# Performance work log

Hardware: AMD Instinct MI355X
Metric: run time of the kernel (lower is better)

Reference implementation:

```python
import jax, jax.numpy as jnp
import numpy as np

B, T, D, H = 8, 512, 1024, 16
DH = D // H  # per-head feature dim (64)


def setup_inputs() -> dict:
    key = jax.random.key(0)
    ks = jax.random.split(key, 10)
    s = 1.0 / np.sqrt(DH)
    inp = {
        "X_data": jax.random.normal(ks[0], (B, T, D), dtype=jnp.float32),
        "mask": jnp.ones((B, T), dtype=jnp.int32),
        # per-head Q/K/V projections (each SelfAttention has its own d_h x d_h weights)
        "Wq": jax.random.normal(ks[1], (H, DH, DH), dtype=jnp.float32) * s,
        "bq": jnp.zeros((H, DH), dtype=jnp.float32),
        "Wk": jax.random.normal(ks[2], (H, DH, DH), dtype=jnp.float32) * s,
        "bk": jnp.zeros((H, DH), dtype=jnp.float32),
        "Wv": jax.random.normal(ks[3], (H, DH, DH), dtype=jnp.float32) * s,
        "bv": jnp.zeros((H, DH), dtype=jnp.float32),
        # AttentionFusion: linear on concatenated head outputs -> len_feature_new
        "Wf": jax.random.normal(ks[4], (D, D), dtype=jnp.float32) * (1.0 / np.sqrt(D)),
        "bf": jnp.zeros((D,), dtype=jnp.float32),
    }
    return inp


def reference(X_data, mask, Wq, bq, Wk, bk, Wv, bv, Wf, bf):
    # Split features into heads: [B, T, H, DH] (equal partitions since D % H == 0)
    Xh = X_data.reshape(B, T, H, DH)
    # Batched per-head projections (replaces the Python loop over heads)
    Q = jnp.einsum("bthd,hde->bhte", Xh, Wq) + bq[None, :, None, :]
    K = jnp.einsum("bthd,hde->bhte", Xh, Wk) + bk[None, :, None, :]
    V = jnp.einsum("bthd,hde->bhte", Xh, Wv) + bv[None, :, None, :]
    scale = 1.0 / jnp.sqrt(jnp.asarray(DH, dtype=Q.dtype))
    scores = jnp.einsum("bhqe,bhke->bhqk", Q, K) * scale  # [B, H, T, T]
    scores = jnp.where(mask[:, None, None, :] > 0, scores, jnp.asarray(-1e9, scores.dtype))
    att = jax.nn.softmax(scores, axis=-1)
    out = jnp.einsum("bhqk,bhke->bhqe", att, V)  # [B, H, T, DH]
    # Concatenate heads (same order as the per-head loop) and fuse
    out = out.transpose(0, 2, 1, 3).reshape(B, T, D)
    fused = out @ Wf + bf  # AttentionFusion linear
    return fused
```

## Files before the change

### kernel.cpp

```cpp
#include <hip/hip_runtime.h>
#include <math.h>

#define B 8
#define T 512
#define D 1024
#define H 16
#define DH 64

typedef __bf16 bf16;
typedef __attribute__((ext_vector_type(8))) __bf16 bf16x8;
typedef __attribute__((ext_vector_type(4))) __bf16 bf16x4;
typedef __attribute__((ext_vector_type(4))) float f32x4;

__device__ __forceinline__ void gld16(const void* g, void* l) {
    __builtin_amdgcn_global_load_lds(
        (const __attribute__((address_space(1))) void*)g,
        (__attribute__((address_space(3))) void*)l, 16, 0, 0);
}


#define EXP2SCALE 1.44269504088896f

__global__ __launch_bounds__(256, 2) void qkv_attn(
    const float* __restrict__ X, const int* __restrict__ mask,
    const float* __restrict__ Wq, const float* __restrict__ Wk,
    const float* __restrict__ Wv,
    const float* __restrict__ bq, const float* __restrict__ bv,
    const float* __restrict__ Wf, bf16* __restrict__ WfT,
    bf16* __restrict__ Ob)
{
    __shared__ __align__(16) char smem[61952];

    if (blockIdx.x >= 512) {
        bf16* Ts = (bf16*)smem;
        const int ti = blockIdx.x - 512, tid = threadIdx.x;
        const int k0 = (ti >> 4) * 64, n0 = (ti & 15) * 64;
        for (int i = tid; i < 1024; i += 256) {
            const int k = i >> 4, nq = (i & 15) * 4;
            const float4 w = *(const float4*)(Wf + (size_t)(k0 + k) * D + n0 + nq);
            Ts[(nq + 0) * 72 + k] = (bf16)w.x; Ts[(nq + 1) * 72 + k] = (bf16)w.y;
            Ts[(nq + 2) * 72 + k] = (bf16)w.z; Ts[(nq + 3) * 72 + k] = (bf16)w.w;
        }
        __syncthreads();
        for (int i = tid; i < 512; i += 256) {
            const int n = i >> 3, kc = (i & 7) * 8;
            *(bf16x8*)(WfT + (size_t)(n0 + n) * D + k0 + kc) = *(const bf16x8*)&Ts[n * 72 + kc];
        }
        return;
    }

    bf16* Wvs  = (bf16*)(smem);
    bf16* Pl   = (bf16*)(smem + 43008);
    int*  msk  = (int*)(smem + 61440);
    bf16* Wqs  = (bf16*)(smem + 8192);
    bf16* WksT = (bf16*)(smem + 24576);
    bf16* Xq   = Pl;
    bf16* Stage = Pl;
    bf16* Ostage = Pl;

    const int bh = blockIdx.x & 127, q0 = (blockIdx.x >> 7) * 128;
    const int b = bh >> 4, h = bh & 15;
    const int tid = threadIdx.x, wave = tid >> 6, lane = tid & 63;
    const int quad = lane >> 4, l15 = lane & 15;

    const int pkrow = wave * 16 + (lane >> 2);
    const int pc0 = (lane & 3) * 2;

    float bqr[4], bvr[4];
#pragma unroll
    for (int nt = 0; nt < 4; ++nt) {
        bqr[nt] = bq[h * DH + nt * 16 + l15];
        bvr[nt] = bv[h * DH + nt * 16 + l15];
    }

    float4 px0, px1, px2, px3;
    {
        const float* src = X + (size_t)(b * T + pkrow) * D + h * DH + pc0 * 8;
        px0 = *(const float4*)src; px1 = *(const float4*)(src + 4);
        px2 = *(const float4*)(src + 8); px3 = *(const float4*)(src + 12);
    }
    int mreg = (tid < 64) ? mask[(size_t)b * T + tid] : 0;

    for (int i = tid; i < 1024; i += 256) {
        const int d = i >> 4, eq4 = (i & 15) * 4;
        const float4 wq4 = *(const float4*)(Wq + (size_t)h * 4096 + d * 64 + eq4);
        const float4 wk4 = *(const float4*)(Wk + (size_t)h * 4096 + d * 64 + eq4);
        const float4 wv4 = *(const float4*)(Wv + (size_t)h * 4096 + d * 64 + eq4);
#pragma unroll
        for (int j = 0; j < 4; ++j) {
            const int e = eq4 + j;
            const int idx = e * 64 + (((d >> 3) ^ (e & 7)) * 8) + (d & 7);
            Wqs[idx] = (bf16)((const float*)&wq4)[j];
            Wvs[idx] = (bf16)((const float*)&wv4)[j];
        }
        bf16x4 wkp;
        wkp[0] = (bf16)wk4.x; wkp[1] = (bf16)wk4.y;
        wkp[2] = (bf16)wk4.z; wkp[3] = (bf16)wk4.w;
        *(bf16x4*)&WksT[d * 64 + (((eq4 >> 3) ^ (d & 7)) * 8) + (eq4 & 7)] = wkp;
    }
    for (int i = tid; i < 1024; i += 256) {
        const int row = i >> 3, c = i & 7;
        const float* src = X + (size_t)(b * T + q0 + row) * D + h * DH + c * 8;
        const float4 x0 = *(const float4*)src;
        const float4 x1 = *(const float4*)(src + 4);
        bf16x8 t;
        t[0] = (bf16)x0.x; t[1] = (bf16)x0.y; t[2] = (bf16)x0.z; t[3] = (bf16)x0.w;
        t[4] = (bf16)x1.x; t[5] = (bf16)x1.y; t[6] = (bf16)x1.z; t[7] = (bf16)x1.w;
        *(bf16x8*)&Xq[row * 64 + ((c ^ (row & 7)) * 8)] = t;
    }
    __syncthreads();

    {
        f32x4 accQ[2][4] = {};
#pragma unroll
        for (int ks = 0; ks < 2; ++ks) {
            bf16x8 af[2], bfr[4];
#pragma unroll
            for (int mt = 0; mt < 2; ++mt) {
                const int row = wave * 32 + mt * 16 + l15;
                af[mt] = *(const bf16x8*)&Xq[row * 64 + (((ks * 4 + quad) ^ (l15 & 7)) * 8)];
            }
#pragma unroll
            for (int nt = 0; nt < 4; ++nt)
                bfr[nt] = *(const bf16x8*)&Wqs[(nt * 16 + l15) * 64 + (((ks * 4 + quad) ^ (l15 & 7)) * 8)];
#pragma unroll
            for (int mt = 0; mt < 2; ++mt)
#pragma unroll
                for (int nt = 0; nt < 4; ++nt)
                    accQ[mt][nt] = __builtin_amdgcn_mfma_f32_16x16x32_bf16(af[mt], bfr[nt], accQ[mt][nt], 0, 0, 0);
        }
        __syncthreads();
        const float qs = 0.125f * EXP2SCALE;
#pragma unroll
        for (int mt = 0; mt < 2; ++mt)
#pragma unroll
            for (int nt = 0; nt < 4; ++nt)
#pragma unroll
                for (int reg = 0; reg < 4; ++reg)
                    Stage[(wave * 32 + mt * 16 + quad * 4 + reg) * 72 + nt * 16 + l15] =
                        (bf16)((accQ[mt][nt][reg] + bqr[nt]) * qs);
        __builtin_amdgcn_wave_barrier();
    }
    bf16x8 qf[2][2];
#pragma unroll
    for (int mt = 0; mt < 2; ++mt)
#pragma unroll
        for (int ks = 0; ks < 2; ++ks)
            qf[mt][ks] = *(const bf16x8*)&Stage[(wave * 32 + mt * 16 + l15) * 72 + ks * 32 + quad * 8];

    bf16x8 qmf[2][2];
    {
        f32x4 accM[2][4] = {};
#pragma unroll
        for (int ks = 0; ks < 2; ++ks)
#pragma unroll
            for (int nt = 0; nt < 4; ++nt) {
                const bf16x8 wk8 = *(const bf16x8*)&WksT[(nt * 16 + l15) * 64 + (((ks * 4 + quad) ^ (l15 & 7)) * 8)];
#pragma unroll
                for (int mt = 0; mt < 2; ++mt)
                    accM[mt][nt] = __builtin_amdgcn_mfma_f32_16x16x32_bf16(wk8, qf[mt][ks], accM[mt][nt], 0, 0, 0);
            }
        __builtin_amdgcn_wave_barrier();
#pragma unroll
        for (int mt = 0; mt < 2; ++mt)
#pragma unroll
            for (int nt = 0; nt < 4; ++nt) {
                bf16x4 qp;
#pragma unroll
                for (int reg = 0; reg < 4; ++reg) qp[reg] = (bf16)accM[mt][nt][reg];
                *(bf16x4*)&Stage[(wave * 32 + mt * 16 + l15) * 72 + nt * 16 + quad * 4] = qp;
            }
        __builtin_amdgcn_wave_barrier();
#pragma unroll
        for (int mt = 0; mt < 2; ++mt)
#pragma unroll
            for (int ks = 0; ks < 2; ++ks)
                qmf[mt][ks] = *(const bf16x8*)&Stage[(wave * 32 + mt * 16 + l15) * 72 + ks * 32 + quad * 8];
    }
    __syncthreads();

    f32x4 acc[2][4] = {};
    float lst2[2] = {0.f, 0.f};

    for (int kt = 0; kt < 8; ++kt) {
        const int p = kt & 1;
        bf16* Xkt = (bf16*)(smem + 8192 + p * 8192);
        bf16* Vts = (bf16*)(smem + 24576 + p * 9216);

        {
            bf16x8 t0, t1;
            t0[0] = (bf16)px0.x; t0[1] = (bf16)px0.y; t0[2] = (bf16)px0.z; t0[3] = (bf16)px0.w;
            t0[4] = (bf16)px1.x; t0[5] = (bf16)px1.y; t0[6] = (bf16)px1.z; t0[7] = (bf16)px1.w;
            t1[0] = (bf16)px2.x; t1[1] = (bf16)px2.y; t1[2] = (bf16)px2.z; t1[3] = (bf16)px2.w;
            t1[4] = (bf16)px3.x; t1[5] = (bf16)px3.y; t1[6] = (bf16)px3.z; t1[7] = (bf16)px3.w;
            *(bf16x8*)&Xkt[pkrow * 64 + ((pc0 ^ (pkrow & 7)) * 8)] = t0;
            *(bf16x8*)&Xkt[pkrow * 64 + (((pc0 + 1) ^ (pkrow & 7)) * 8)] = t1;
            if (tid < 64) msk[p * 64 + tid] = mreg;
        }
        __builtin_amdgcn_wave_barrier();

        if (kt < 7) {
            const float* src = X + (size_t)(b * T + (kt + 1) * 64 + pkrow) * D + h * DH + pc0 * 8;
            px0 = *(const float4*)src; px1 = *(const float4*)(src + 4);
            px2 = *(const float4*)(src + 8); px3 = *(const float4*)(src + 12);
            if (tid < 64) mreg = mask[(size_t)b * T + (kt + 1) * 64 + tid];
        }

        {
            bf16x8 afkv[2];
#pragma unroll
            for (int ks = 0; ks < 2; ++ks)
                afkv[ks] = *(const bf16x8*)&Xkt[(wave * 16 + l15) * 64 + (((ks * 4 + quad) ^ (l15 & 7)) * 8)];
            f32x4 accV[4] = {};
            __builtin_amdgcn_s_setprio(1);
#pragma unroll
            for (int ks = 0; ks < 2; ++ks)
#pragma unroll
                for (int nt = 0; nt < 4; ++nt) {
                    const bf16x8 bv8 = *(const bf16x8*)&Wvs[(nt * 16 + l15) * 64 + (((ks * 4 + quad) ^ (l15 & 7)) * 8)];
                    accV[nt] = __builtin_amdgcn_mfma_f32_16x16x32_bf16(afkv[ks], bv8, accV[nt], 0, 0, 0);
                }
            __builtin_amdgcn_s_setprio(0);
#pragma unroll
            for (int nt = 0; nt < 4; ++nt) {
                bf16x4 vp;
#pragma unroll
                for (int reg = 0; reg < 4; ++reg) vp[reg] = (bf16)accV[nt][reg];
                *(bf16x4*)&Vts[(nt * 16 + l15) * 72 + wave * 16 + quad * 4] = vp;
            }
        }
        asm volatile("s_waitcnt lgkmcnt(0)" ::: "memory");
        __builtin_amdgcn_s_barrier();

        bf16* Plw = Pl + wave * (32 * 72);
        {
            bf16x8 xkf[4][2];
#pragma unroll
            for (int nt = 0; nt < 4; ++nt)
#pragma unroll
                for (int ks = 0; ks < 2; ++ks)
                    xkf[nt][ks] = *(const bf16x8*)&Xkt[(nt * 16 + l15) * 64 + (((ks * 4 + quad) ^ (l15 & 7)) * 8)];
            int4 mv4[4];
#pragma unroll
            for (int nt = 0; nt < 4; ++nt)
                mv4[nt] = *(const int4*)&msk[p * 64 + nt * 16 + quad * 4];
#pragma unroll
            for (int mt = 0; mt < 2; ++mt) {
                f32x4 s[4] = {};
                __builtin_amdgcn_s_setprio(1);
#pragma unroll
                for (int ks = 0; ks < 2; ++ks)
#pragma unroll
                    for (int nt = 0; nt < 4; ++nt)
                        s[nt] = __builtin_amdgcn_mfma_f32_16x16x32_bf16(xkf[nt][ks], qmf[mt][ks], s[nt], 0, 0, 0);
                __builtin_amdgcn_s_setprio(0);
#pragma unroll
                for (int nt = 0; nt < 4; ++nt) {
                    bf16x4 pp;
                    const float p0 = (mv4[nt].x > 0) ? exp2f(s[nt][0]) : 0.f;
                    const float p1 = (mv4[nt].y > 0) ? exp2f(s[nt][1]) : 0.f;
                    const float p2 = (mv4[nt].z > 0) ? exp2f(s[nt][2]) : 0.f;
                    const float p3 = (mv4[nt].w > 0) ? exp2f(s[nt][3]) : 0.f;
                    lst2[mt] += (p0 + p1) + (p2 + p3);
                    pp[0] = (bf16)p0; pp[1] = (bf16)p1; pp[2] = (bf16)p2; pp[3] = (bf16)p3;
                    *(bf16x4*)&Plw[(mt * 16 + l15) * 72 + nt * 16 + quad * 4] = pp;
                }
            }
        }
        __builtin_amdgcn_wave_barrier();

        __builtin_amdgcn_s_setprio(1);
#pragma unroll
        for (int kc = 0; kc < 2; ++kc) {
            const bf16x8 pf0 = *(const bf16x8*)&Plw[(l15) * 72 + kc * 32 + quad * 8];
            const bf16x8 pf1 = *(const bf16x8*)&Plw[(16 + l15) * 72 + kc * 32 + quad * 8];
#pragma unroll
            for (int nt = 0; nt < 4; ++nt) {
                const bf16x8 vf = *(const bf16x8*)&Vts[(nt * 16 + l15) * 72 + kc * 32 + quad * 8];
                acc[0][nt] = __builtin_amdgcn_mfma_f32_16x16x32_bf16(pf0, vf, acc[0][nt], 0, 0, 0);
                acc[1][nt] = __builtin_amdgcn_mfma_f32_16x16x32_bf16(pf1, vf, acc[1][nt], 0, 0, 0);
            }
        }
        __builtin_amdgcn_s_setprio(0);
    }

    __builtin_amdgcn_wave_barrier();
    float inv_r[2][4];
#pragma unroll
    for (int mt = 0; mt < 2; ++mt) {
        float l = lst2[mt];
        l += __shfl_xor(l, 16);
        l += __shfl_xor(l, 32);
        const float inv = 1.f / l;
#pragma unroll
        for (int reg = 0; reg < 4; ++reg)
            inv_r[mt][reg] = __shfl(inv, (lane & 48) | (quad * 4 + reg));
    }
#pragma unroll
    for (int mt = 0; mt < 2; ++mt)
#pragma unroll
        for (int reg = 0; reg < 4; ++reg) {
            const int row = wave * 32 + mt * 16 + quad * 4 + reg;
#pragma unroll
            for (int nt = 0; nt < 4; ++nt)
                Ostage[row * 72 + nt * 16 + l15] =
                    (bf16)(acc[mt][nt][reg] * inv_r[mt][reg] + bvr[nt]);
        }
    __syncthreads();
    for (int i = tid; i < 1024; i += 256) {
        const int row = i >> 3, c = (i & 7) * 8;
        *(bf16x8*)(Ob + ((size_t)b * T + q0 + row) * D + h * DH + c) =
            *(const bf16x8*)&Ostage[row * 72 + c];
    }
}

__global__ __launch_bounds__(512, 4) void fuse_mfma(
    const bf16* __restrict__ Ob, const bf16* __restrict__ WfT,
    const float* __restrict__ bfv, float* __restrict__ out)
{
    __shared__ __align__(16) char smem[73728];

    const int col0 = blockIdx.x * 64;
    const int row0 = blockIdx.y * 128;
    const int tid = threadIdx.x, wave = tid >> 6, lane = tid & 63;
    const int quad = lane >> 4, l15 = lane & 15;
    const int lr = lane >> 3, lc = lane & 7;
    const int wm = (wave >> 1) * 32, wn = (wave & 1) * 32;

    f32x4 acc[2][2] = {};

    auto stage = [&](int t) {
        const int buf = t - (t / 3) * 3;
        bf16* As = (bf16*)(smem + buf * 24576);
        bf16* Bs = (bf16*)(smem + buf * 24576 + 16384);
        const int k0 = t * 64;
#pragma unroll
        for (int j = 0; j < 2; ++j) {
            const int row = wave * 16 + j * 8 + lr;
            gld16(Ob + (size_t)(row0 + row) * D + k0 + ((lc ^ (row & 7)) * 8),
                  &As[(wave * 16 + j * 8) * 64]);
        }
        const int rowB = wave * 8 + lr;
        gld16(WfT + (size_t)(col0 + rowB) * D + k0 + ((lc ^ (rowB & 7)) * 8),
              &Bs[(wave * 8) * 64]);
    };

    stage(0);
    stage(1);

    for (int i = 0; i < 16; ++i) {
        if (i < 15) asm volatile("s_waitcnt vmcnt(3)" ::: "memory");
        else        asm volatile("s_waitcnt vmcnt(0)" ::: "memory");
        __builtin_amdgcn_s_barrier();

        const int buf = i - (i / 3) * 3;
        bf16* As = (bf16*)(smem + buf * 24576);
        bf16* Bs = (bf16*)(smem + buf * 24576 + 16384);
#pragma unroll
        for (int ks = 0; ks < 2; ++ks) {
            bf16x8 af[2], bfr[2];
#pragma unroll
            for (int mt = 0; mt < 2; ++mt)
                af[mt] = *(const bf16x8*)&As[(wm + mt * 16 + l15) * 64 + (((ks * 4 + quad) ^ (l15 & 7)) * 8)];
#pragma unroll
            for (int nt = 0; nt < 2; ++nt)
                bfr[nt] = *(const bf16x8*)&Bs[(wn + nt * 16 + l15) * 64 + (((ks * 4 + quad) ^ (l15 & 7)) * 8)];
#pragma unroll
            for (int mt = 0; mt < 2; ++mt)
#pragma unroll
                for (int nt = 0; nt < 2; ++nt)
                    acc[mt][nt] = __builtin_amdgcn_mfma_f32_16x16x32_bf16(af[mt], bfr[nt], acc[mt][nt], 0, 0, 0);
        }
        if (i < 14) stage(i + 2);
    }
    __syncthreads();

    float* Ofs = (float*)smem;
    float bias[2];
#pragma unroll
    for (int nt = 0; nt < 2; ++nt) bias[nt] = bfv[col0 + wn + nt * 16 + l15];
#pragma unroll
    for (int mt = 0; mt < 2; ++mt)
#pragma unroll
        for (int reg = 0; reg < 4; ++reg) {
            const int row = wm + mt * 16 + quad * 4 + reg;
#pragma unroll
            for (int nt = 0; nt < 2; ++nt)
                Ofs[row * 68 + wn + nt * 16 + l15] = acc[mt][nt][reg] + bias[nt];
        }
    __syncthreads();
    for (int i = tid; i < 2048; i += 512) {
        const int row = i >> 4, c = (i & 15) * 4;
        *(float4*)(out + (size_t)(row0 + row) * D + col0 + c) = *(const float4*)&Ofs[row * 68 + c];
    }
}

extern "C" void kernel_launch(void* const* d_in, const int* in_sizes, int n_in,
                              void* d_out, int out_size, void* d_ws, size_t ws_size,
                              hipStream_t stream) {
    const float* X   = (const float*)d_in[0];
    const int* mask  = (const int*)d_in[1];
    const float* Wq  = (const float*)d_in[2];
    const float* bq  = (const float*)d_in[3];
    const float* Wk  = (const float*)d_in[4];
    const float* bk  = (const float*)d_in[5];
    const float* Wv  = (const float*)d_in[6];
    const float* bv  = (const float*)d_in[7];
    const float* Wf  = (const float*)d_in[8];
    const float* bfv = (const float*)d_in[9];
    float* out = (float*)d_out;
    (void)bk;

    bf16* wsb = (bf16*)d_ws;
    const size_t QN = (size_t)B * H * T * DH;
    bf16* Ob  = wsb;
    bf16* WfT = wsb + QN;

    qkv_attn<<<dim3(768), 256, 0, stream>>>(X, mask, Wq, Wk, Wv, bq, bv, Wf, WfT, Ob);
    fuse_mfma<<<dim3(D / 64, (B * T) / 128), 512, 0, stream>>>(Ob, WfT, bfv, out);
}
```

Before: 122.3 us.

## Load mask directly into registers, reorder transpose blocks first, add setprio in GEMM

```diff
diff --git a/kernel.cpp b/kernel.cpp
--- a/kernel.cpp
+++ b/kernel.cpp
@@ -29,11 +29,11 @@
     const float* __restrict__ Wf, bf16* __restrict__ WfT,
     bf16* __restrict__ Ob)
 {
-    __shared__ __align__(16) char smem[61952];
-
-    if (blockIdx.x >= 512) {
+    __shared__ __align__(16) char smem[61440];
+
+    if (blockIdx.x < 256) {
         bf16* Ts = (bf16*)smem;
-        const int ti = blockIdx.x - 512, tid = threadIdx.x;
+        const int ti = blockIdx.x, tid = threadIdx.x;
         const int k0 = (ti >> 4) * 64, n0 = (ti & 15) * 64;
         for (int i = tid; i < 1024; i += 256) {
             const int k = i >> 4, nq = (i & 15) * 4;
@@ -51,14 +51,14 @@
 
     bf16* Wvs  = (bf16*)(smem);
     bf16* Pl   = (bf16*)(smem + 43008);
-    int*  msk  = (int*)(smem + 61440);
     bf16* Wqs  = (bf16*)(smem + 8192);
     bf16* WksT = (bf16*)(smem + 24576);
     bf16* Xq   = Pl;
     bf16* Stage = Pl;
     bf16* Ostage = Pl;
 
-    const int bh = blockIdx.x & 127, q0 = (blockIdx.x >> 7) * 128;
+    const int abid = blockIdx.x - 256;
+    const int bh = abid & 127, q0 = (abid >> 7) * 128;
     const int b = bh >> 4, h = bh & 15;
     const int tid = threadIdx.x, wave = tid >> 6, lane = tid & 63;
     const int quad = lane >> 4, l15 = lane & 15;
@@ -79,7 +79,10 @@
         px0 = *(const float4*)src; px1 = *(const float4*)(src + 4);
         px2 = *(const float4*)(src + 8); px3 = *(const float4*)(src + 12);
     }
-    int mreg = (tid < 64) ? mask[(size_t)b * T + tid] : 0;
+    int4 mvc[4], mvn[4];
+#pragma unroll
+    for (int nt = 0; nt < 4; ++nt)
+        mvc[nt] = *(const int4*)&mask[(size_t)b * T + nt * 16 + quad * 4];
 
     for (int i = tid; i < 1024; i += 256) {
         const int d = i >> 4, eq4 = (i & 15) * 4;
@@ -195,7 +198,6 @@
             t1[4] = (bf16)px3.x; t1[5] = (bf16)px3.y; t1[6] = (bf16)px3.z; t1[7] = (bf16)px3.w;
             *(bf16x8*)&Xkt[pkrow * 64 + ((pc0 ^ (pkrow & 7)) * 8)] = t0;
             *(bf16x8*)&Xkt[pkrow * 64 + (((pc0 + 1) ^ (pkrow & 7)) * 8)] = t1;
-            if (tid < 64) msk[p * 64 + tid] = mreg;
         }
         __builtin_amdgcn_wave_barrier();
 
@@ -203,7 +205,9 @@
             const float* src = X + (size_t)(b * T + (kt + 1) * 64 + pkrow) * D + h * DH + pc0 * 8;
             px0 = *(const float4*)src; px1 = *(const float4*)(src + 4);
             px2 = *(const float4*)(src + 8); px3 = *(const float4*)(src + 12);
-            if (tid < 64) mreg = mask[(size_t)b * T + (kt + 1) * 64 + tid];
+#pragma unroll
+            for (int nt = 0; nt < 4; ++nt)
+                mvn[nt] = *(const int4*)&mask[(size_t)b * T + (kt + 1) * 64 + nt * 16 + quad * 4];
         }
 
         {
@@ -240,10 +244,6 @@
 #pragma unroll
                 for (int ks = 0; ks < 2; ++ks)
                     xkf[nt][ks] = *(const bf16x8*)&Xkt[(nt * 16 + l15) * 64 + (((ks * 4 + quad) ^ (l15 & 7)) * 8)];
-            int4 mv4[4];
-#pragma unroll
-            for (int nt = 0; nt < 4; ++nt)
-                mv4[nt] = *(const int4*)&msk[p * 64 + nt * 16 + quad * 4];
 #pragma unroll
             for (int mt = 0; mt < 2; ++mt) {
                 f32x4 s[4] = {};
@@ -257,10 +257,10 @@
 #pragma unroll
                 for (int nt = 0; nt < 4; ++nt) {
                     bf16x4 pp;
-                    const float p0 = (mv4[nt].x > 0) ? exp2f(s[nt][0]) : 0.f;
-                    const float p1 = (mv4[nt].y > 0) ? exp2f(s[nt][1]) : 0.f;
-                    const float p2 = (mv4[nt].z > 0) ? exp2f(s[nt][2]) : 0.f;
-                    const float p3 = (mv4[nt].w > 0) ? exp2f(s[nt][3]) : 0.f;
+                    const float p0 = (mvc[nt].x > 0) ? exp2f(s[nt][0]) : 0.f;
+                    const float p1 = (mvc[nt].y > 0) ? exp2f(s[nt][1]) : 0.f;
+                    const float p2 = (mvc[nt].z > 0) ? exp2f(s[nt][2]) : 0.f;
+                    const float p3 = (mvc[nt].w > 0) ? exp2f(s[nt][3]) : 0.f;
                     lst2[mt] += (p0 + p1) + (p2 + p3);
                     pp[0] = (bf16)p0; pp[1] = (bf16)p1; pp[2] = (bf16)p2; pp[3] = (bf16)p3;
                     *(bf16x4*)&Plw[(mt * 16 + l15) * 72 + nt * 16 + quad * 4] = pp;
@@ -282,6 +282,8 @@
             }
         }
         __builtin_amdgcn_s_setprio(0);
+#pragma unroll
+        for (int nt = 0; nt < 4; ++nt) mvc[nt] = mvn[nt];
     }
 
     __builtin_amdgcn_wave_barrier();
@@ -356,6 +358,7 @@
         const int buf = i - (i / 3) * 3;
         bf16* As = (bf16*)(smem + buf * 24576);
         bf16* Bs = (bf16*)(smem + buf * 24576 + 16384);
+        __builtin_amdgcn_s_setprio(1);
 #pragma unroll
         for (int ks = 0; ks < 2; ++ks) {
             bf16x8 af[2], bfr[2];
@@ -371,6 +374,7 @@
                 for (int nt = 0; nt < 2; ++nt)
                     acc[mt][nt] = __builtin_amdgcn_mfma_f32_16x16x32_bf16(af[mt], bfr[nt], acc[mt][nt], 0, 0, 0);
         }
+        __builtin_amdgcn_s_setprio(0);
         if (i < 14) stage(i + 2);
     }
     __syncthreads();
```

Result: no change. 124.2 us (+1.6%).
